# Performance work log

Measured on AMD Instinct MI355X. Metric: run time of the kernel, lower is better.

Reference implementation:

```python
import jax, jax.numpy as jnp
import numpy as np

BATCH = 2048
BUCKETS = 100000
DIM = 64

def setup_inputs() -> dict:
    key = jax.random.key(0)
    k1, k2 = jax.random.split(key)
    inputs = jax.random.uniform(k1, (BATCH, BUCKETS), dtype=jnp.float32)
    embeddings = jax.random.normal(k2, (BUCKETS, DIM), dtype=jnp.float32)
    return {"inputs": inputs, "embeddings": embeddings}

def reference(inputs, embeddings):
    # K.dot(inputs, embeddings): [B, buckets] @ [buckets, dim] -> [B, dim]
    out = jnp.matmul(inputs, embeddings)
    # mean=True branch: divide by count of active buckets, zero where empty
    s = jnp.sum(inputs, axis=-1, keepdims=True)  # [B, 1]
    out = jnp.where(s > 0, out / s, jnp.zeros_like(out))
    return out
```

## Files before the change

kernel.cpp:

```cpp
#include <hip/hip_runtime.h>
#include <hip/hip_bf16.h>

#define BATCH 2048
#define KDIM  100000
#define DIM   64
#define NKB   (KDIM / 32)
#define KP    16
#define NRB   32
#define SS    4
#define NSS   49

typedef __attribute__((ext_vector_type(8))) short  short8;
typedef __attribute__((ext_vector_type(4))) float  f32x4;

__device__ __forceinline__ unsigned short f2bf(float f) {
    union { float f; unsigned int u; } v; v.f = f;
    unsigned int u = v.u;
    u += 0x7FFFu + ((u >> 16) & 1u);
    return (unsigned short)(u >> 16);
}

__device__ __forceinline__ void glds16(const float* src, unsigned char* lds) {
    __builtin_amdgcn_global_load_lds(
        (const __attribute__((address_space(1))) void*)src,
        (__attribute__((address_space(3))) void*)lds, 16, 0, 0);
}

__global__ __launch_bounds__(256)
void hashemb_pack(const float* __restrict__ emb, unsigned short* __restrict__ pB) {
    const int kb   = blockIdx.x;
    const int t    = threadIdx.x >> 6;
    const int lane = threadIdx.x & 63;
    const int col  = t * 16 + (lane & 15);
    const int krow = kb * 32 + (lane >> 4) * 8;

    short8 w;
    #pragma unroll
    for (int j = 0; j < 8; ++j)
        w[j] = (short)f2bf(emb[(size_t)(krow + j) * DIM + col]);

    *(short8*)&pB[(((size_t)kb * 4 + t) * 64 + lane) * 8] = w;
}

__global__ __launch_bounds__(256, 2)
void hashemb_matmul(const float* __restrict__ inp,
                    const unsigned short* __restrict__ pB,
                    float* __restrict__ part,
                    float* __restrict__ rsp) {
    __shared__ __align__(1024) unsigned char smem[4][2][8192];

    const int tid  = threadIdx.x;
    const int lane = tid & 63;
    const int wid  = tid >> 6;

    const int wg  = blockIdx.x;
    const int xcd = wg & 7;
    const int pos = wg >> 3;
    const int kp  = xcd * 2 + (pos >> 5);
    const int rb  = pos & 31;

    const int cbase = NKB / KP;
    const int rem   = NKB % KP;
    const int cnt   = cbase + (kp < rem ? 1 : 0);
    const int kb0   = kp * cbase + (kp < rem ? kp : rem);
    const int kbEnd = kb0 + cnt;

    const int rowbase = rb * 64 + wid * 16;

    const int rsub = lane >> 5;
    const int gcol = lane & 31;
    const int frow = lane & 15;
    const int g    = lane >> 4;
    const int sw   = lane & 7;

    const float* srcrow[8];
    #pragma unroll
    for (int i = 0; i < 8; ++i) {
        const int r = 2 * i + rsub;
        srcrow[i] = inp + (size_t)(rowbase + r) * KDIM + ((gcol ^ (r & 7)) << 2);
    }

    unsigned char* cur = &smem[wid][0][0];
    unsigned char* nxt = &smem[wid][1][0];

    auto ssStart = [&](int s) {
        int b = kb0 + s * SS;
        return (b > NKB - SS) ? (NKB - SS) : b;
    };
    auto issue = [&](int base, unsigned char* buf) {
        #pragma unroll
        for (int i = 0; i < 8; ++i)
            glds16(srcrow[i] + (size_t)base * 32, buf + i * 1024);
    };

    f32x4 acc[4];
    #pragma unroll
    for (int t = 0; t < 4; ++t) acc[t] = (f32x4)0.0f;
    float lsum = 0.0f;

    issue(kb0, cur);

    for (int s = 0; s < NSS; ++s) {
        const int base = ssStart(s);
        const int lo   = kb0 + s * SS;

        short8 Br[4][4];
        #pragma unroll
        for (int q = 0; q < SS; ++q) {
            const unsigned short* bq = pB + (size_t)(base + q) * 2048 + (size_t)lane * 8;
            #pragma unroll
            for (int t = 0; t < 4; ++t)
                Br[q][t] = *(const short8*)(bq + t * 512);
        }
        __builtin_amdgcn_sched_barrier(0);

        if (s + 1 < NSS) {
            issue(ssStart(s + 1), nxt);
            asm volatile("s_waitcnt vmcnt(8)" ::: "memory");
        } else {
            asm volatile("s_waitcnt vmcnt(0)" ::: "memory");
        }
        __builtin_amdgcn_sched_barrier(0);

        #pragma unroll
        for (int q = 0; q < SS; ++q) {
            const int c = base + q;
            if (c >= lo && c < kbEnd) {
                const int jb = (q << 3) + (g << 1);
                const f32x4 xa = *(const f32x4*)(cur + frow * 512 + (((jb    ) ^ sw) << 4));
                const f32x4 xb = *(const f32x4*)(cur + frow * 512 + (((jb + 1) ^ sw) << 4));
                short8 af;
                #pragma unroll
                for (int j = 0; j < 4; ++j) {
                    af[j]     = (short)f2bf(xa[j]);
                    af[4 + j] = (short)f2bf(xb[j]);
                }
                lsum += xa[0] + xa[1] + xa[2] + xa[3]
                      + xb[0] + xb[1] + xb[2] + xb[3];
                #pragma unroll
                for (int t = 0; t < 4; ++t)
                    acc[t] = __builtin_amdgcn_mfma_f32_16x16x32_bf16(af, Br[q][t], acc[t], 0, 0, 0);
            }
        }

        unsigned char* tmp = cur; cur = nxt; nxt = tmp;
    }

    lsum += __shfl_xor(lsum, 16, 64);
    lsum += __shfl_xor(lsum, 32, 64);
    if (lane < 16) rsp[(size_t)kp * BATCH + rowbase + lane] = lsum;

    float* po = part + (size_t)kp * BATCH * DIM;
    #pragma unroll
    for (int t = 0; t < 4; ++t) {
        const int col = t * 16 + frow;
        #pragma unroll
        for (int j = 0; j < 4; ++j) {
            const int row = rowbase + g * 4 + j;
            po[(size_t)row * DIM + col] = acc[t][j];
        }
    }
}

__global__ __launch_bounds__(256)
void hashemb_rsreduce(const float* __restrict__ rsp, float* __restrict__ rs) {
    const int row = blockIdx.x * 256 + threadIdx.x;
    float s = 0.0f;
    #pragma unroll
    for (int p = 0; p < KP; ++p) s += rsp[(size_t)p * BATCH + row];
    rs[row] = s;
}

__global__ __launch_bounds__(256)
void hashemb_finalize(const float* __restrict__ part, const float* __restrict__ rs,
                      float* __restrict__ out) {
    const int i4 = blockIdx.x * 256 + threadIdx.x;
    const float s = rs[i4 >> 4];
    f32x4 o = (f32x4)0.0f;
    #pragma unroll
    for (int p = 0; p < KP; ++p)
        o += *(const f32x4*)(part + (size_t)p * BATCH * DIM + (size_t)i4 * 4);
    const float inv = (s > 0.0f) ? (1.0f / s) : 0.0f;
    o *= inv;
    *(f32x4*)(out + (size_t)i4 * 4) = o;
}

extern "C" void kernel_launch(void* const* d_in, const int* in_sizes, int n_in,
                              void* d_out, int out_size, void* d_ws, size_t ws_size,
                              hipStream_t stream) {
    const float* inp = (const float*)d_in[0];
    const float* emb = (const float*)d_in[1];
    float* out = (float*)d_out;

    float* rs   = (float*)d_ws;
    float* rsp  = (float*)((char*)d_ws + 8192);
    float* part = (float*)((char*)d_ws + 139264);
    unsigned short* pB = (unsigned short*)((char*)d_ws + 8527872);

    hashemb_pack<<<NKB, 256, 0, stream>>>(emb, pB);

    hashemb_matmul<<<NRB * KP, 256, 0, stream>>>(inp, pB, part, rsp);

    hashemb_rsreduce<<<BATCH / 256, 256, 0, stream>>>(rsp, rs);

    hashemb_finalize<<<(BATCH * DIM / 4) / 256, 256, 0, stream>>>(part, rs, out);
}
```

Before: 212.7 us.

## Restructure split-K matmul into 16-row tiles with shared LDS staging across waves

Each workgroup now covers 16 rows and one of 8 K-splits, instead of 64 rows and one of 16 K-splits. The four waves share one double-buffered 16-row by 16-K-block LDS tile, and each wave processes a different 4-block K slice, so there are now 32 partial slices per row. This adds workgroup barriers per stage. The row-sum reduction kernel is folded into finalize, which now sums 32 partials instead of 16, doubling the partial-buffer traffic. The intent is to get larger contiguous loads per row and fewer launches, at the cost of extra synchronisation and larger partial buffers.

Result: slower. 222.0 us (+4.4%).

```diff
diff --git a/kernel.cpp b/kernel.cpp
--- a/kernel.cpp
+++ b/kernel.cpp
@@ -5,10 +5,11 @@
 #define KDIM  100000
 #define DIM   64
 #define NKB   (KDIM / 32)
-#define KP    16
-#define NRB   32
-#define SS    4
-#define NSS   49
+#define KP    8
+#define TS    16
+#define NSS   25
+#define NRT   (BATCH / 16)
+#define NSL   (KP * 4)
 
 typedef __attribute__((ext_vector_type(8))) short  short8;
 typedef __attribute__((ext_vector_type(4))) float  f32x4;
@@ -39,7 +40,7 @@
     for (int j = 0; j < 8; ++j)
         w[j] = (short)f2bf(emb[(size_t)(krow + j) * DIM + col]);
 
-    *(short8*)&pB[(((size_t)kb * 4 + t) * 64 + lane) * 8] = w;
+    *(short8*)&pB[(size_t)kb * 2048 + t * 512 + (size_t)lane * 8] = w;
 }
 
 __global__ __launch_bounds__(256, 2)
@@ -47,50 +48,44 @@
                     const unsigned short* __restrict__ pB,
                     float* __restrict__ part,
                     float* __restrict__ rsp) {
-    __shared__ __align__(1024) unsigned char smem[4][2][8192];
+    __shared__ __align__(1024) unsigned char smem[2][16 * 2048];
 
     const int tid  = threadIdx.x;
     const int lane = tid & 63;
     const int wid  = tid >> 6;
 
-    const int wg  = blockIdx.x;
-    const int xcd = wg & 7;
-    const int pos = wg >> 3;
-    const int kp  = xcd * 2 + (pos >> 5);
-    const int rb  = pos & 31;
-
-    const int cbase = NKB / KP;
-    const int rem   = NKB % KP;
-    const int cnt   = cbase + (kp < rem ? 1 : 0);
-    const int kb0   = kp * cbase + (kp < rem ? kp : rem);
+    const int wg = blockIdx.x;
+    const int kp = wg & 7;
+    const int rb = wg >> 3;
+
+    const int cnt   = 390 + (kp < 5 ? 1 : 0);
+    const int kb0   = kp * 390 + (kp < 5 ? kp : 5);
     const int kbEnd = kb0 + cnt;
 
-    const int rowbase = rb * 64 + wid * 16;
-
-    const int rsub = lane >> 5;
-    const int gcol = lane & 31;
+    const int rowbase = rb * 16;
     const int frow = lane & 15;
     const int g    = lane >> 4;
-    const int sw   = lane & 7;
-
-    const float* srcrow[8];
+    const int sw   = frow & 7;
+
+    const float* srcp[8];
+    int dst[8];
     #pragma unroll
     for (int i = 0; i < 8; ++i) {
-        const int r = 2 * i + rsub;
-        srcrow[i] = inp + (size_t)(rowbase + r) * KDIM + ((gcol ^ (r & 7)) << 2);
+        const int rl = wid * 4 + (i >> 1);
+        const int h  = i & 1;
+        srcp[i] = inp + (size_t)(rowbase + rl) * KDIM + h * 256 + ((lane ^ (rl & 7)) << 2);
+        dst[i]  = rl * 2048 + h * 1024;
     }
 
-    unsigned char* cur = &smem[wid][0][0];
-    unsigned char* nxt = &smem[wid][1][0];
-
-    auto ssStart = [&](int s) {
-        int b = kb0 + s * SS;
-        return (b > NKB - SS) ? (NKB - SS) : b;
+    auto tb = [&](int s) {
+        int b = kb0 + s * TS;
+        const int m = kbEnd - TS;
+        return (b > m) ? m : b;
     };
     auto issue = [&](int base, unsigned char* buf) {
         #pragma unroll
         for (int i = 0; i < 8; ++i)
-            glds16(srcrow[i] + (size_t)base * 32, buf + i * 1024);
+            glds16(srcp[i] + (size_t)base * 32, buf + dst[i]);
     };
 
     f32x4 acc[4];
@@ -98,37 +93,44 @@
     for (int t = 0; t < 4; ++t) acc[t] = (f32x4)0.0f;
     float lsum = 0.0f;
 
-    issue(kb0, cur);
+    unsigned char* cur = &smem[0][0];
+    unsigned char* nxt = &smem[1][0];
+    issue(tb(0), cur);
+
+    const int rdb = frow * 2048 + ((((g << 1)) ^ sw) << 4);
 
     for (int s = 0; s < NSS; ++s) {
-        const int base = ssStart(s);
-        const int lo   = kb0 + s * SS;
+        const int base = tb(s);
+        const int lo   = kb0 + s * TS;
+        const int cw   = base + wid * 4;
 
         short8 Br[4][4];
         #pragma unroll
-        for (int q = 0; q < SS; ++q) {
-            const unsigned short* bq = pB + (size_t)(base + q) * 2048 + (size_t)lane * 8;
+        for (int qq = 0; qq < 4; ++qq) {
+            const unsigned short* bq = pB + (size_t)(cw + qq) * 2048 + (size_t)lane * 8;
             #pragma unroll
             for (int t = 0; t < 4; ++t)
-                Br[q][t] = *(const short8*)(bq + t * 512);
+                Br[qq][t] = *(const short8*)(bq + t * 512);
         }
         __builtin_amdgcn_sched_barrier(0);
 
         if (s + 1 < NSS) {
-            issue(ssStart(s + 1), nxt);
+            issue(tb(s + 1), nxt);
+            __builtin_amdgcn_sched_barrier(0);
             asm volatile("s_waitcnt vmcnt(8)" ::: "memory");
         } else {
             asm volatile("s_waitcnt vmcnt(0)" ::: "memory");
         }
-        __builtin_amdgcn_sched_barrier(0);
-
-        #pragma unroll
-        for (int q = 0; q < SS; ++q) {
-            const int c = base + q;
+        __builtin_amdgcn_s_barrier();
+        __builtin_amdgcn_sched_barrier(0);
+
+        #pragma unroll
+        for (int qq = 0; qq < 4; ++qq) {
+            const int c = cw + qq;
             if (c >= lo && c < kbEnd) {
-                const int jb = (q << 3) + (g << 1);
-                const f32x4 xa = *(const f32x4*)(cur + frow * 512 + (((jb    ) ^ sw) << 4));
-                const f32x4 xb = *(const f32x4*)(cur + frow * 512 + (((jb + 1) ^ sw) << 4));
+                const int off = (wid * 4 + qq) * 128 + rdb;
+                const f32x4 xa = *(const f32x4*)(cur + off);
+                const f32x4 xb = *(const f32x4*)(cur + (off ^ 16));
                 short8 af;
                 #pragma unroll
                 for (int j = 0; j < 4; ++j) {
@@ -139,18 +141,24 @@
                       + xb[0] + xb[1] + xb[2] + xb[3];
                 #pragma unroll
                 for (int t = 0; t < 4; ++t)
-                    acc[t] = __builtin_amdgcn_mfma_f32_16x16x32_bf16(af, Br[q][t], acc[t], 0, 0, 0);
+                    acc[t] = __builtin_amdgcn_mfma_f32_16x16x32_bf16(af, Br[qq][t], acc[t], 0, 0, 0);
             }
         }
+        __builtin_amdgcn_sched_barrier(0);
+        asm volatile("s_waitcnt lgkmcnt(0)" ::: "memory");
+        __builtin_amdgcn_s_barrier();
+        __builtin_amdgcn_sched_barrier(0);
 
         unsigned char* tmp = cur; cur = nxt; nxt = tmp;
     }
 
+    const int sl = kp * 4 + wid;
+
     lsum += __shfl_xor(lsum, 16, 64);
     lsum += __shfl_xor(lsum, 32, 64);
-    if (lane < 16) rsp[(size_t)kp * BATCH + rowbase + lane] = lsum;
-
-    float* po = part + (size_t)kp * BATCH * DIM;
+    if (lane < 16) rsp[(size_t)sl * BATCH + rowbase + lane] = lsum;
+
+    float* po = part + (size_t)sl * BATCH * DIM;
     #pragma unroll
     for (int t = 0; t < 4; ++t) {
         const int col = t * 16 + frow;
@@ -163,23 +171,20 @@
 }
 
 __global__ __launch_bounds__(256)
-void hashemb_rsreduce(const float* __restrict__ rsp, float* __restrict__ rs) {
-    const int row = blockIdx.x * 256 + threadIdx.x;
+void hashemb_finalize(const float* __restrict__ part, const float* __restrict__ rsp,
+                      float* __restrict__ out) {
+    const int i4  = blockIdx.x * 256 + threadIdx.x;
+    const int row = i4 >> 4;
+
     float s = 0.0f;
     #pragma unroll
-    for (int p = 0; p < KP; ++p) s += rsp[(size_t)p * BATCH + row];
-    rs[row] = s;
-}
-
-__global__ __launch_bounds__(256)
-void hashemb_finalize(const float* __restrict__ part, const float* __restrict__ rs,
-                      float* __restrict__ out) {
-    const int i4 = blockIdx.x * 256 + threadIdx.x;
-    const float s = rs[i4 >> 4];
+    for (int p = 0; p < NSL; ++p) s += rsp[(size_t)p * BATCH + row];
+
     f32x4 o = (f32x4)0.0f;
     #pragma unroll
-    for (int p = 0; p < KP; ++p)
+    for (int p = 0; p < NSL; ++p)
         o += *(const f32x4*)(part + (size_t)p * BATCH * DIM + (size_t)i4 * 4);
+
     const float inv = (s > 0.0f) ? (1.0f / s) : 0.0f;
     o *= inv;
     *(f32x4*)(out + (size_t)i4 * 4) = o;
@@ -192,16 +197,13 @@
     const float* emb = (const float*)d_in[1];
     float* out = (float*)d_out;
 
-    float* rs   = (float*)d_ws;
-    float* rsp  = (float*)((char*)d_ws + 8192);
-    float* part = (float*)((char*)d_ws + 139264);
-    unsigned short* pB = (unsigned short*)((char*)d_ws + 8527872);
+    float* rsp  = (float*)d_ws;
+    float* part = (float*)((char*)d_ws + 262144);
+    unsigned short* pB = (unsigned short*)((char*)d_ws + 17039360);
 
     hashemb_pack<<<NKB, 256, 0, stream>>>(emb, pB);
 
-    hashemb_matmul<<<NRB * KP, 256, 0, stream>>>(inp, pB, part, rsp);
-
-    hashemb_rsreduce<<<BATCH / 256, 256, 0, stream>>>(rsp, rs);
-
-    hashemb_finalize<<<(BATCH * DIM / 4) / 256, 256, 0, stream>>>(part, rs, out);
-}
+    hashemb_matmul<<<NRT * KP, 256, 0, stream>>>(inp, pB, part, rsp);
+
+    hashemb_finalize<<<(BATCH * DIM / 4) / 256, 256, 0, stream>>>(part, rsp, out);
+}
```
